# Optimization experiments

Measured on AMD Instinct MI355X. Metric: run time of the kernel, lower is better.

Reference implementation:

```python
import jax, jax.numpy as jnp
import numpy as np

DIM_V = 1024
H = 16
D = DIM_V // H
EPS = 1e-5


def _ln(x, g, b):
    m = jnp.mean(x, axis=-1, keepdims=True)
    v = jnp.var(x, axis=-1, keepdims=True)
    return (x - m) * jax.lax.rsqrt(v + EPS) * g + b


def setup_inputs() -> dict:
    key = jax.random.key(0)
    ks = jax.random.split(key, 8)
    B, Nq, Nk = 4, 1024, 1024
    s = 1.0 / np.sqrt(DIM_V)
    return {
        "Q": jax.random.normal(ks[0], (B, Nq, DIM_V), jnp.float32),
        "K": jax.random.normal(ks[1], (B, Nk, DIM_V), jnp.float32),
        "structure_bias": jax.random.normal(ks[2], (H, B, Nq, Nk), jnp.float32) * 0.1,
        "Wq": jax.random.normal(ks[3], (DIM_V, DIM_V), jnp.float32) * s,
        "bq": jnp.zeros((DIM_V,), jnp.float32),
        "Wk": jax.random.normal(ks[4], (DIM_V, DIM_V), jnp.float32) * s,
        "bk": jnp.zeros((DIM_V,), jnp.float32),
        "Wv": jax.random.normal(ks[5], (DIM_V, DIM_V), jnp.float32) * s,
        "bv": jnp.zeros((DIM_V,), jnp.float32),
        "Wo": jax.random.normal(ks[6], (DIM_V, DIM_V), jnp.float32) * s,
        "bo": jnp.zeros((DIM_V,), jnp.float32),
        "gamma0": jnp.ones((DIM_V,), jnp.float32),
        "beta0": jnp.zeros((DIM_V,), jnp.float32),
        "gamma1": jnp.ones((DIM_V,), jnp.float32),
        "beta1": jnp.zeros((DIM_V,), jnp.float32),
    }


def reference(Q, K, structure_bias, Wq, bq, Wk, bk, Wv, bv, Wo, bo,
              gamma0, beta0, gamma1, beta1):
    B, Nq, _ = Q.shape
    Nk = K.shape[1]
    q = Q @ Wq.T + bq                      # [B,Nq,dV]
    k = K @ Wk.T + bk                      # [B,Nk,dV]
    v = K @ Wv.T + bv                      # [B,Nk,dV]
    # torch cat(split(d_head,2),0) => head-major leading axis; use [H,B,N,D]
    qh = q.reshape(B, Nq, H, D).transpose(2, 0, 1, 3)
    kh = k.reshape(B, Nk, H, D).transpose(2, 0, 1, 3)
    vh = v.reshape(B, Nk, H, D).transpose(2, 0, 1, 3)
    # NOTE: scale by sqrt(dim_V), not sqrt(d_head) — faithful to source
    A = jnp.einsum('hbqd,hbkd->hbqk', qh, kh) / jnp.sqrt(jnp.float32(DIM_V))
    A = jax.nn.softmax(A + structure_bias, axis=-1)
    oh = qh + jnp.einsum('hbqk,hbkd->hbqd', A, vh)   # residual on Q_
    O = oh.transpose(1, 2, 0, 3).reshape(B, Nq, DIM_V)
    O = _ln(O, gamma0, beta0)
    O = O + jax.nn.relu(O @ Wo.T + bo)     # dropout is identity in eval
    O = _ln(O, gamma1, beta1)
    return O
```

## Files before the change

kernel.cpp:

```cpp
#include <hip/hip_runtime.h>

using s8v = __attribute__((ext_vector_type(8))) short;
using s4v = __attribute__((ext_vector_type(4))) short;
using f4v = __attribute__((ext_vector_type(4))) float;
using bf8v = __attribute__((ext_vector_type(8))) __bf16;

__device__ __forceinline__ short f2b(float f) {
  __bf16 h = (__bf16)f;
  return __builtin_bit_cast(short, h);
}

__device__ __forceinline__ f4v mfma16(s8v a, s8v b, f4v c) {
  return __builtin_amdgcn_mfma_f32_16x16x32_bf16(
      __builtin_bit_cast(bf8v, a), __builtin_bit_cast(bf8v, b), c, 0, 0, 0);
}

__device__ __forceinline__ void glds16(const void* src, void* dst) {
  __builtin_amdgcn_global_load_lds(
      (const __attribute__((address_space(1))) void*)src,
      (__attribute__((address_space(3))) void*)dst, 16, 0, 0);
}

__global__ __launch_bounds__(256) void cast_kernel(
    const float* __restrict__ Q, const float* __restrict__ K,
    const float* __restrict__ Wq, const float* __restrict__ Wk,
    const float* __restrict__ Wv, const float* __restrict__ Wo,
    short* __restrict__ Qb, short* __restrict__ Kb,
    short* __restrict__ Wqb, short* __restrict__ Wkb,
    short* __restrict__ Wvb, short* __restrict__ Wob) {
  int bi = blockIdx.x;
  const float* src; short* dst; int off;
  if (bi < 2048)      { src = Q;  dst = Qb;  off = bi; }
  else if (bi < 4096) { src = K;  dst = Kb;  off = bi - 2048; }
  else if (bi < 4608) { src = Wq; dst = Wqb; off = bi - 4096; }
  else if (bi < 5120) { src = Wk; dst = Wkb; off = bi - 4608; }
  else if (bi < 5632) { src = Wv; dst = Wvb; off = bi - 5120; }
  else                { src = Wo; dst = Wob; off = bi - 5632; }
  size_t base = (size_t)off * 2048 + threadIdx.x * 8;
  f4v a = *(const f4v*)(src + base);
  f4v b = *(const f4v*)(src + base + 4);
  s8v o8;
#pragma unroll
  for (int j = 0; j < 4; ++j) { o8[j] = f2b(a[j]); o8[4 + j] = f2b(b[j]); }
  *(s8v*)(dst + base) = o8;
}

__device__ __forceinline__ void gemm_core(const short* __restrict__ A,
                                          const short* __restrict__ W,
                                          f4v acc[4][4], short* As, short* Ws,
                                          int tm, int tn, int tid) {
  const int lane = tid & 63, wid = tid >> 6;
  const int c = lane & 15, g = lane >> 4;
  const int wr = wid >> 1, wc = wid & 1;
  for (int kb = 0; kb < 16; ++kb) {
    __syncthreads();
#pragma unroll
    for (int p = 0; p < 4; ++p) {
      int row = p * 32 + wid * 8 + (lane >> 3);
      int chunk = (lane & 7) ^ (row & 7);
      glds16(A + (size_t)(tm + row) * 1024 + kb * 64 + chunk * 8,
             As + p * 2048 + wid * 512);
      glds16(W + (size_t)(tn + row) * 1024 + kb * 64 + chunk * 8,
             Ws + p * 2048 + wid * 512);
    }
    asm volatile("s_waitcnt vmcnt(0)" ::: "memory");
    __syncthreads();
#pragma unroll
    for (int ks = 0; ks < 2; ++ks) {
      s8v af[4], wf[4];
#pragma unroll
      for (int i = 0; i < 4; ++i) {
        int ra = wr * 64 + i * 16 + c;
        af[i] = *(const s8v*)(As + ra * 64 + ((((ks << 2) + g) ^ (ra & 7)) << 3));
        int rb = wc * 64 + i * 16 + c;
        wf[i] = *(const s8v*)(Ws + rb * 64 + ((((ks << 2) + g) ^ (rb & 7)) << 3));
      }
#pragma unroll
      for (int i = 0; i < 4; ++i)
#pragma unroll
        for (int j = 0; j < 4; ++j)
          acc[i][j] = mfma16(af[i], wf[j], acc[i][j]);
    }
  }
}

__global__ __launch_bounds__(256, 2) void gemm_proj(
    const short* __restrict__ Qb, const short* __restrict__ Kb,
    const short* __restrict__ Wqb, const short* __restrict__ Wkb,
    const short* __restrict__ Wvb, const float* __restrict__ bq,
    const float* __restrict__ bk, const float* __restrict__ bv,
    float* __restrict__ qws, short* __restrict__ khs, short* __restrict__ vts) {
  __shared__ short As[8192], Ws[8192];
  const int tid = threadIdx.x, lane = tid & 63, wid = tid >> 6;
  const int c = lane & 15, g = lane >> 4;
  const int wr = wid >> 1, wc = wid & 1;
  const int tm = blockIdx.y * 128, tn = blockIdx.x * 128;
  const int z = blockIdx.z;
  const short* A = (z == 0) ? Qb : Kb;
  const short* W = (z == 0) ? Wqb : ((z == 1) ? Wkb : Wvb);
  const float* bias = (z == 0) ? bq : ((z == 1) ? bk : bv);
  f4v acc[4][4] = {};
  gemm_core(A, W, acc, As, Ws, tm, tn, tid);
#pragma unroll
  for (int j = 0; j < 4; ++j) {
    const int o = tn + wc * 64 + j * 16 + c;
    const float bj = bias[o];
    const int h = o >> 6, d = o & 63;
#pragma unroll
    for (int i = 0; i < 4; ++i) {
      const int m0 = tm + wr * 64 + i * 16 + g * 4;
      if (z == 0) {
#pragma unroll
        for (int r = 0; r < 4; ++r)
          qws[(size_t)(m0 + r) * 1024 + o] = acc[i][j][r] + bj;
      } else if (z == 1) {
        const int bidx = m0 >> 10;
#pragma unroll
        for (int r = 0; r < 4; ++r) {
          int n = (m0 + r) & 1023;
          khs[((size_t)(h * 4 + bidx) * 1024 + n) * 64 + d] =
              f2b(acc[i][j][r] + bj);
        }
      } else {
        const int bidx = m0 >> 10, n0 = m0 & 1023;
        s4v pk;
#pragma unroll
        for (int r = 0; r < 4; ++r) pk[r] = f2b(acc[i][j][r] + bj);
        *(s4v*)(vts + ((size_t)(h * 4 + bidx) * 64 + d) * 1024 + n0) = pk;
      }
    }
  }
}

__global__ __launch_bounds__(256, 2) void gemm_out(
    const short* __restrict__ t0b, const short* __restrict__ Wob,
    const float* __restrict__ bo, const float* __restrict__ res,
    float* __restrict__ O2) {
  __shared__ short As[8192], Ws[8192];
  const int tid = threadIdx.x, lane = tid & 63, wid = tid >> 6;
  const int c = lane & 15, g = lane >> 4;
  const int wr = wid >> 1, wc = wid & 1;
  const int tm = blockIdx.y * 128, tn = blockIdx.x * 128;
  f4v acc[4][4] = {};
  gemm_core(t0b, Wob, acc, As, Ws, tm, tn, tid);
#pragma unroll
  for (int j = 0; j < 4; ++j) {
    const int o = tn + wc * 64 + j * 16 + c;
    const float bj = bo[o];
#pragma unroll
    for (int i = 0; i < 4; ++i) {
      const int m0 = tm + wr * 64 + i * 16 + g * 4;
#pragma unroll
      for (int r = 0; r < 4; ++r) {
        size_t idx = (size_t)(m0 + r) * 1024 + o;
        float y = acc[i][j][r] + bj;
        y = fmaxf(y, 0.f);
        O2[idx] = res[idx] + y;
      }
    }
  }
}

__global__ __launch_bounds__(256, 2) void attn_kernel(
    const short* __restrict__ khs, const short* __restrict__ vts,
    const float* __restrict__ qf, const float* __restrict__ sb,
    float* __restrict__ o_attn) {
  const int tid = threadIdx.x, wid = tid >> 6, lane = tid & 63;
  const int c = lane & 15, g = lane >> 4;
  const int hb = blockIdx.y, h = hb >> 2, b = hb & 3;
  const int qw = blockIdx.x * 128 + wid * 32;

  __shared__ short Ks[64 * 64];
  __shared__ short Vs[64 * 64];
  __shared__ short Ps[4 * 32 * 72];

  const short* kb_base = khs + (size_t)hb * 65536;
  const short* vb_base = vts + (size_t)hb * 65536;
  const float* sb_base = sb + (size_t)hb * 1048576;

  s8v qb[2][2];
#pragma unroll
  for (int nf = 0; nf < 2; ++nf)
#pragma unroll
    for (int ks = 0; ks < 2; ++ks) {
      const float* qp = qf + ((size_t)(b * 1024 + qw + nf * 16 + c)) * 1024 +
                        h * 64 + ks * 32 + g * 8;
      f4v lo = *(const f4v*)qp;
      f4v hi = *(const f4v*)(qp + 4);
      s8v t;
#pragma unroll
      for (int j = 0; j < 4; ++j) { t[j] = f2b(lo[j]); t[4 + j] = f2b(hi[j]); }
      qb[nf][ks] = t;
    }

  float m_run[2] = {-3.0e38f, -3.0e38f};
  float l_run[2] = {0.f, 0.f};
  f4v oacc[2][4] = {};

  for (int kb = 0; kb < 16; ++kb) {
    __syncthreads();
#pragma unroll
    for (int p = 0; p < 2; ++p) {
      int row = p * 32 + wid * 8 + (lane >> 3);
      int chunk = (lane & 7) ^ (row & 7);
      glds16(kb_base + (size_t)(kb * 64 + row) * 64 + chunk * 8,
             Ks + p * 2048 + wid * 512);
      glds16(vb_base + (size_t)row * 1024 + kb * 64 + chunk * 8,
             Vs + p * 2048 + wid * 512);
    }
    asm volatile("s_waitcnt vmcnt(0)" ::: "memory");
    __syncthreads();

    f4v accs[4][2] = {};
#pragma unroll
    for (int ks = 0; ks < 2; ++ks) {
      s8v kf[4];
#pragma unroll
      for (int mf = 0; mf < 4; ++mf) {
        int row = mf * 16 + c;
        kf[mf] = *(const s8v*)(Ks + row * 64 +
                               ((((ks << 2) + g) ^ (row & 7)) << 3));
      }
#pragma unroll
      for (int mf = 0; mf < 4; ++mf)
#pragma unroll
        for (int nf = 0; nf < 2; ++nf)
          accs[mf][nf] = mfma16(kf[mf], qb[nf][ks], accs[mf][nf]);
    }

    float alpha_s[2];
#pragma unroll
    for (int nf = 0; nf < 2; ++nf) {
      const int q = qw + nf * 16 + c;
      const float* bp0 = sb_base + (size_t)q * 1024 + kb * 64 + g * 4;
      float tmax = -3.0e38f;
#pragma unroll
      for (int mf = 0; mf < 4; ++mf) {
        f4v bb = *(const f4v*)(bp0 + mf * 16);
        f4v x = accs[mf][nf] * 0.03125f + bb;
        accs[mf][nf] = x;
        tmax = fmaxf(tmax, fmaxf(fmaxf(x[0], x[1]), fmaxf(x[2], x[3])));
      }
      tmax = fmaxf(tmax, __shfl_xor(tmax, 16));
      tmax = fmaxf(tmax, __shfl_xor(tmax, 32));
      const float mn = fmaxf(m_run[nf], tmax);
      const float al = __expf(m_run[nf] - mn);
      float ssum = 0.f;
#pragma unroll
      for (int mf = 0; mf < 4; ++mf) {
        f4v x = accs[mf][nf];
        float p0 = __expf(x[0] - mn), p1 = __expf(x[1] - mn);
        float p2 = __expf(x[2] - mn), p3 = __expf(x[3] - mn);
        ssum += (p0 + p1) + (p2 + p3);
        s4v pk;
        pk[0] = f2b(p0); pk[1] = f2b(p1); pk[2] = f2b(p2); pk[3] = f2b(p3);
        *(s4v*)(Ps + (size_t)wid * 2304 + (size_t)(nf * 16 + c) * 72 +
                mf * 16 + g * 4) = pk;
      }
      ssum += __shfl_xor(ssum, 16);
      ssum += __shfl_xor(ssum, 32);
      l_run[nf] = l_run[nf] * al + ssum;
      m_run[nf] = mn;
      alpha_s[nf] = al;
    }

#pragma unroll
    for (int mfq = 0; mfq < 2; ++mfq) {
      float a0 = __shfl(alpha_s[mfq], g * 4 + 0);
      float a1 = __shfl(alpha_s[mfq], g * 4 + 1);
      float a2 = __shfl(alpha_s[mfq], g * 4 + 2);
      float a3 = __shfl(alpha_s[mfq], g * 4 + 3);
#pragma unroll
      for (int nd = 0; nd < 4; ++nd) {
        oacc[mfq][nd][0] *= a0; oacc[mfq][nd][1] *= a1;
        oacc[mfq][nd][2] *= a2; oacc[mfq][nd][3] *= a3;
      }
    }

#pragma unroll
    for (int ks2 = 0; ks2 < 2; ++ks2) {
      s8v pf[2], vf[4];
#pragma unroll
      for (int mfq = 0; mfq < 2; ++mfq)
        pf[mfq] = *(const s8v*)(Ps + (size_t)wid * 2304 +
                                (size_t)(mfq * 16 + c) * 72 + ks2 * 32 + g * 8);
#pragma unroll
      for (int nd = 0; nd < 4; ++nd) {
        int d = nd * 16 + c;
        vf[nd] = *(const s8v*)(Vs + d * 64 +
                               ((((ks2 << 2) + g) ^ (d & 7)) << 3));
      }
#pragma unroll
      for (int mfq = 0; mfq < 2; ++mfq)
#pragma unroll
        for (int nd = 0; nd < 4; ++nd)
          oacc[mfq][nd] = mfma16(pf[mfq], vf[nd], oacc[mfq][nd]);
    }
  }

#pragma unroll
  for (int mfq = 0; mfq < 2; ++mfq) {
    float i0 = 1.f / __shfl(l_run[mfq], g * 4 + 0);
    float i1 = 1.f / __shfl(l_run[mfq], g * 4 + 1);
    float i2 = 1.f / __shfl(l_run[mfq], g * 4 + 2);
    float i3 = 1.f / __shfl(l_run[mfq], g * 4 + 3);
#pragma unroll
    for (int nd = 0; nd < 4; ++nd) {
      int d = nd * 16 + c;
      size_t base = ((size_t)(b * 1024 + qw + mfq * 16 + g * 4)) * 1024 +
                    h * 64 + d;
      o_attn[base]        = qf[base]        + oacc[mfq][nd][0] * i0;
      o_attn[base + 1024] = qf[base + 1024] + oacc[mfq][nd][1] * i1;
      o_attn[base + 2048] = qf[base + 2048] + oacc[mfq][nd][2] * i2;
      o_attn[base + 3072] = qf[base + 3072] + oacc[mfq][nd][3] * i3;
    }
  }
}

template <bool WB>
__global__ __launch_bounds__(256) void ln_k(const float* __restrict__ in,
                                            float* __restrict__ out,
                                            short* __restrict__ outb,
                                            const float* __restrict__ gamma,
                                            const float* __restrict__ beta) {
  const int row = blockIdx.x, tid = threadIdx.x;
  const size_t base = (size_t)row * 1024 + tid * 4;
  f4v x = *(const f4v*)(in + base);
  float s = (x[0] + x[1]) + (x[2] + x[3]);
  float ss = (x[0] * x[0] + x[1] * x[1]) + (x[2] * x[2] + x[3] * x[3]);
#pragma unroll
  for (int m = 1; m < 64; m <<= 1) {
    s += __shfl_xor(s, m);
    ss += __shfl_xor(ss, m);
  }
  __shared__ float red[8];
  const int wid = tid >> 6, lane = tid & 63;
  if (lane == 0) { red[wid] = s; red[4 + wid] = ss; }
  __syncthreads();
  s = (red[0] + red[1]) + (red[2] + red[3]);
  ss = (red[4] + red[5]) + (red[6] + red[7]);
  const float mean = s * (1.f / 1024.f);
  const float var = ss * (1.f / 1024.f) - mean * mean;
  const float rs = rsqrtf(var + 1e-5f);
  const f4v gg = *(const f4v*)(gamma + tid * 4);
  const f4v bb = *(const f4v*)(beta + tid * 4);
  f4v y;
#pragma unroll
  for (int jj = 0; jj < 4; ++jj) y[jj] = (x[jj] - mean) * rs * gg[jj] + bb[jj];
  *(f4v*)(out + base) = y;
  if (WB) {
    s4v pk;
#pragma unroll
    for (int jj = 0; jj < 4; ++jj) pk[jj] = f2b(y[jj]);
    *(s4v*)(outb + base) = pk;
  }
}

extern "C" void kernel_launch(void* const* d_in, const int* in_sizes, int n_in,
                              void* d_out, int out_size, void* d_ws,
                              size_t ws_size, hipStream_t stream) {
  const float* Q  = (const float*)d_in[0];
  const float* K  = (const float*)d_in[1];
  const float* sb = (const float*)d_in[2];
  const float* Wq = (const float*)d_in[3];
  const float* bq = (const float*)d_in[4];
  const float* Wk = (const float*)d_in[5];
  const float* bk = (const float*)d_in[6];
  const float* Wv = (const float*)d_in[7];
  const float* bv = (const float*)d_in[8];
  const float* Wo = (const float*)d_in[9];
  const float* bo = (const float*)d_in[10];
  const float* g0 = (const float*)d_in[11];
  const float* b0 = (const float*)d_in[12];
  const float* g1 = (const float*)d_in[13];
  const float* b1 = (const float*)d_in[14];
  float* out = (float*)d_out;

  char* ws = (char*)d_ws;
  size_t off = 0;
  auto alloc = [&](size_t bytes) -> void* {
    void* p = ws + off;
    off += (bytes + 255) & ~(size_t)255;
    return p;
  };
  float* qws  = (float*)alloc((size_t)16 << 20);
  short* khs  = (short*)alloc((size_t)8 << 20);
  short* vts  = (short*)alloc((size_t)8 << 20);
  short* Qb   = (short*)alloc((size_t)8 << 20);
  short* Kb   = (short*)alloc((size_t)8 << 20);
  short* Wqb  = (short*)alloc((size_t)2 << 20);
  short* Wkb  = (short*)alloc((size_t)2 << 20);
  short* Wvb  = (short*)alloc((size_t)2 << 20);
  short* Wob  = (short*)alloc((size_t)2 << 20);
  float* oat  = (float*)alloc((size_t)16 << 20);
  short* t0b  = (short*)alloc((size_t)8 << 20);
  float* O2   = qws;

  cast_kernel<<<6144, 256, 0, stream>>>(Q, K, Wq, Wk, Wv, Wo, Qb, Kb, Wqb, Wkb,
                                        Wvb, Wob);
  gemm_proj<<<dim3(8, 32, 3), 256, 0, stream>>>(Qb, Kb, Wqb, Wkb, Wvb, bq, bk,
                                                bv, qws, khs, vts);
  attn_kernel<<<dim3(8, 64), 256, 0, stream>>>(khs, vts, qws, sb, oat);
  ln_k<true><<<4096, 256, 0, stream>>>(oat, oat, t0b, g0, b0);
  gemm_out<<<dim3(8, 32), 256, 0, stream>>>(t0b, Wob, bo, oat, O2);
  ln_k<false><<<4096, 256, 0, stream>>>(O2, out, nullptr, g1, b1);
}
```

Measured before the change: 543.8 us.

## Double-buffer LDS tiles in GEMMs and attention, prefetch bias, remap blocks across XCDs

GEMM and attention kernels now double-buffer their LDS tiles, issuing the next tile's global-to-LDS loads before computing on the current tile. The attention kernel also prefetches the next structure-bias block into registers. Block indices are remapped so neighbouring tiles land on the same XCD for better L2 reuse. This targets exposed global memory latency, at the cost of more LDS and registers per block, which may lower occupancy.

Result: faster. 529.5 us (-2.6%).

```diff
diff --git a/kernel.cpp b/kernel.cpp
--- a/kernel.cpp
+++ b/kernel.cpp
@@ -45,43 +45,65 @@
   *(s8v*)(dst + base) = o8;
 }
 
-__device__ __forceinline__ void gemm_core(const short* __restrict__ A,
-                                          const short* __restrict__ W,
-                                          f4v acc[4][4], short* As, short* Ws,
-                                          int tm, int tn, int tid) {
+__device__ __forceinline__ void stage_tile(const short* __restrict__ A,
+                                           const short* __restrict__ W,
+                                           short* As, short* Ws, int tm, int tn,
+                                           int kb, int tid) {
+  const int lane = tid & 63, wid = tid >> 6;
+#pragma unroll
+  for (int p = 0; p < 4; ++p) {
+    int row = p * 32 + wid * 8 + (lane >> 3);
+    int chunk = (lane & 7) ^ (row & 7);
+    glds16(A + (size_t)(tm + row) * 1024 + kb * 64 + chunk * 8,
+           As + p * 2048 + wid * 512);
+    glds16(W + (size_t)(tn + row) * 1024 + kb * 64 + chunk * 8,
+           Ws + p * 2048 + wid * 512);
+  }
+}
+
+__device__ __forceinline__ void gemm_core_db(const short* __restrict__ A,
+                                             const short* __restrict__ W,
+                                             f4v acc[4][4], short* As, short* Ws,
+                                             int tm, int tn, int tid) {
   const int lane = tid & 63, wid = tid >> 6;
   const int c = lane & 15, g = lane >> 4;
   const int wr = wid >> 1, wc = wid & 1;
+  stage_tile(A, W, As, Ws, tm, tn, 0, tid);
+  asm volatile("s_waitcnt vmcnt(0)" ::: "memory");
+  __syncthreads();
   for (int kb = 0; kb < 16; ++kb) {
-    __syncthreads();
-#pragma unroll
-    for (int p = 0; p < 4; ++p) {
-      int row = p * 32 + wid * 8 + (lane >> 3);
-      int chunk = (lane & 7) ^ (row & 7);
-      glds16(A + (size_t)(tm + row) * 1024 + kb * 64 + chunk * 8,
-             As + p * 2048 + wid * 512);
-      glds16(W + (size_t)(tn + row) * 1024 + kb * 64 + chunk * 8,
-             Ws + p * 2048 + wid * 512);
+    const int cur = kb & 1;
+    short* Asc = As + cur * 8192;
+    short* Wsc = Ws + cur * 8192;
+    if (kb < 15)
+      stage_tile(A, W, As + (cur ^ 1) * 8192, Ws + (cur ^ 1) * 8192, tm, tn,
+                 kb + 1, tid);
+#pragma unroll
+    for (int ks = 0; ks < 2; ++ks) {
+      s8v af[4], wf[4];
+#pragma unroll
+      for (int i = 0; i < 4; ++i) {
+        int ra = wr * 64 + i * 16 + c;
+        af[i] = *(const s8v*)(Asc + ra * 64 + ((((ks << 2) + g) ^ (ra & 7)) << 3));
+        int rb = wc * 64 + i * 16 + c;
+        wf[i] = *(const s8v*)(Wsc + rb * 64 + ((((ks << 2) + g) ^ (rb & 7)) << 3));
+      }
+#pragma unroll
+      for (int i = 0; i < 4; ++i)
+#pragma unroll
+        for (int j = 0; j < 4; ++j)
+          acc[i][j] = mfma16(af[i], wf[j], acc[i][j]);
     }
     asm volatile("s_waitcnt vmcnt(0)" ::: "memory");
     __syncthreads();
-#pragma unroll
-    for (int ks = 0; ks < 2; ++ks) {
-      s8v af[4], wf[4];
-#pragma unroll
-      for (int i = 0; i < 4; ++i) {
-        int ra = wr * 64 + i * 16 + c;
-        af[i] = *(const s8v*)(As + ra * 64 + ((((ks << 2) + g) ^ (ra & 7)) << 3));
-        int rb = wc * 64 + i * 16 + c;
-        wf[i] = *(const s8v*)(Ws + rb * 64 + ((((ks << 2) + g) ^ (rb & 7)) << 3));
-      }
-#pragma unroll
-      for (int i = 0; i < 4; ++i)
-#pragma unroll
-        for (int j = 0; j < 4; ++j)
-          acc[i][j] = mfma16(af[i], wf[j], acc[i][j]);
-    }
-  }
+  }
+}
+
+__device__ __forceinline__ void xcd_remap_gemm(int* tm, int* tn) {
+  int d = blockIdx.y * 8 + blockIdx.x;
+  int o = (d & 7) * 32 + (d >> 3);
+  *tm = (o >> 3) * 128;
+  *tn = (o & 7) * 128;
 }
 
 __global__ __launch_bounds__(256, 2) void gemm_proj(
@@ -90,17 +112,18 @@
     const short* __restrict__ Wvb, const float* __restrict__ bq,
     const float* __restrict__ bk, const float* __restrict__ bv,
     float* __restrict__ qws, short* __restrict__ khs, short* __restrict__ vts) {
-  __shared__ short As[8192], Ws[8192];
+  __shared__ short As[16384], Ws[16384];
   const int tid = threadIdx.x, lane = tid & 63, wid = tid >> 6;
   const int c = lane & 15, g = lane >> 4;
   const int wr = wid >> 1, wc = wid & 1;
-  const int tm = blockIdx.y * 128, tn = blockIdx.x * 128;
+  int tm, tn;
+  xcd_remap_gemm(&tm, &tn);
   const int z = blockIdx.z;
   const short* A = (z == 0) ? Qb : Kb;
   const short* W = (z == 0) ? Wqb : ((z == 1) ? Wkb : Wvb);
   const float* bias = (z == 0) ? bq : ((z == 1) ? bk : bv);
   f4v acc[4][4] = {};
-  gemm_core(A, W, acc, As, Ws, tm, tn, tid);
+  gemm_core_db(A, W, acc, As, Ws, tm, tn, tid);
 #pragma unroll
   for (int j = 0; j < 4; ++j) {
     const int o = tn + wc * 64 + j * 16 + c;
@@ -136,13 +159,14 @@
     const short* __restrict__ t0b, const short* __restrict__ Wob,
     const float* __restrict__ bo, const float* __restrict__ res,
     float* __restrict__ O2) {
-  __shared__ short As[8192], Ws[8192];
+  __shared__ short As[16384], Ws[16384];
   const int tid = threadIdx.x, lane = tid & 63, wid = tid >> 6;
   const int c = lane & 15, g = lane >> 4;
   const int wr = wid >> 1, wc = wid & 1;
-  const int tm = blockIdx.y * 128, tn = blockIdx.x * 128;
+  int tm, tn;
+  xcd_remap_gemm(&tm, &tn);
   f4v acc[4][4] = {};
-  gemm_core(t0b, Wob, acc, As, Ws, tm, tn, tid);
+  gemm_core_db(t0b, Wob, acc, As, Ws, tm, tn, tid);
 #pragma unroll
   for (int j = 0; j < 4; ++j) {
     const int o = tn + wc * 64 + j * 16 + c;
@@ -167,11 +191,13 @@
     float* __restrict__ o_attn) {
   const int tid = threadIdx.x, wid = tid >> 6, lane = tid & 63;
   const int c = lane & 15, g = lane >> 4;
-  const int hb = blockIdx.y, h = hb >> 2, b = hb & 3;
-  const int qw = blockIdx.x * 128 + wid * 32;
-
-  __shared__ short Ks[64 * 64];
-  __shared__ short Vs[64 * 64];
+  const int dlin = blockIdx.y * 8 + blockIdx.x;
+  const int o = (dlin & 7) * 64 + (dlin >> 3);
+  const int hb = o >> 3, h = hb >> 2, b = hb & 3;
+  const int qw = (o & 7) * 128 + wid * 32;
+
+  __shared__ short Ks[2 * 4096];
+  __shared__ short Vs[2 * 4096];
   __shared__ short Ps[4 * 32 * 72];
 
   const short* kb_base = khs + (size_t)hb * 65536;
@@ -193,23 +219,49 @@
       qb[nf][ks] = t;
     }
 
-  float m_run[2] = {-3.0e38f, -3.0e38f};
-  float l_run[2] = {0.f, 0.f};
-  f4v oacc[2][4] = {};
-
-  for (int kb = 0; kb < 16; ++kb) {
-    __syncthreads();
+  auto stage_kv = [&](int buf, int kb) {
 #pragma unroll
     for (int p = 0; p < 2; ++p) {
       int row = p * 32 + wid * 8 + (lane >> 3);
       int chunk = (lane & 7) ^ (row & 7);
       glds16(kb_base + (size_t)(kb * 64 + row) * 64 + chunk * 8,
-             Ks + p * 2048 + wid * 512);
+             Ks + buf * 4096 + p * 2048 + wid * 512);
       glds16(vb_base + (size_t)row * 1024 + kb * 64 + chunk * 8,
-             Vs + p * 2048 + wid * 512);
-    }
-    asm volatile("s_waitcnt vmcnt(0)" ::: "memory");
-    __syncthreads();
+             Vs + buf * 4096 + p * 2048 + wid * 512);
+    }
+  };
+
+  float m_run[2] = {-3.0e38f, -3.0e38f};
+  float l_run[2] = {0.f, 0.f};
+  f4v oacc[2][4] = {};
+
+  stage_kv(0, 0);
+  f4v bc[2][4];
+#pragma unroll
+  for (int nf = 0; nf < 2; ++nf) {
+    const float* bp0 =
+        sb_base + (size_t)(qw + nf * 16 + c) * 1024 + g * 4;
+#pragma unroll
+    for (int mf = 0; mf < 4; ++mf) bc[nf][mf] = *(const f4v*)(bp0 + mf * 16);
+  }
+  asm volatile("s_waitcnt vmcnt(0)" ::: "memory");
+  __syncthreads();
+
+  for (int kb = 0; kb < 16; ++kb) {
+    const int cur = kb & 1;
+    const short* Ksc = Ks + cur * 4096;
+    const short* Vsc = Vs + cur * 4096;
+    if (kb < 15) stage_kv(cur ^ 1, kb + 1);
+    f4v bn[2][4];
+    if (kb < 15) {
+#pragma unroll
+      for (int nf = 0; nf < 2; ++nf) {
+        const float* bp0 = sb_base + (size_t)(qw + nf * 16 + c) * 1024 +
+                           (kb + 1) * 64 + g * 4;
+#pragma unroll
+        for (int mf = 0; mf < 4; ++mf) bn[nf][mf] = *(const f4v*)(bp0 + mf * 16);
+      }
+    }
 
     f4v accs[4][2] = {};
 #pragma unroll
@@ -218,7 +270,7 @@
 #pragma unroll
       for (int mf = 0; mf < 4; ++mf) {
         int row = mf * 16 + c;
-        kf[mf] = *(const s8v*)(Ks + row * 64 +
+        kf[mf] = *(const s8v*)(Ksc + row * 64 +
                                ((((ks << 2) + g) ^ (row & 7)) << 3));
       }
 #pragma unroll
@@ -231,13 +283,10 @@
     float alpha_s[2];
 #pragma unroll
     for (int nf = 0; nf < 2; ++nf) {
-      const int q = qw + nf * 16 + c;
-      const float* bp0 = sb_base + (size_t)q * 1024 + kb * 64 + g * 4;
       float tmax = -3.0e38f;
 #pragma unroll
       for (int mf = 0; mf < 4; ++mf) {
-        f4v bb = *(const f4v*)(bp0 + mf * 16);
-        f4v x = accs[mf][nf] * 0.03125f + bb;
+        f4v x = accs[mf][nf] * 0.03125f + bc[nf][mf];
         accs[mf][nf] = x;
         tmax = fmaxf(tmax, fmaxf(fmaxf(x[0], x[1]), fmaxf(x[2], x[3])));
       }
@@ -287,7 +336,7 @@
 #pragma unroll
       for (int nd = 0; nd < 4; ++nd) {
         int d = nd * 16 + c;
-        vf[nd] = *(const s8v*)(Vs + d * 64 +
+        vf[nd] = *(const s8v*)(Vsc + d * 64 +
                                ((((ks2 << 2) + g) ^ (d & 7)) << 3));
       }
 #pragma unroll
@@ -295,6 +344,15 @@
 #pragma unroll
         for (int nd = 0; nd < 4; ++nd)
           oacc[mfq][nd] = mfma16(pf[mfq], vf[nd], oacc[mfq][nd]);
+    }
+
+    asm volatile("s_waitcnt vmcnt(0)" ::: "memory");
+    __syncthreads();
+    if (kb < 15) {
+#pragma unroll
+      for (int nf = 0; nf < 2; ++nf)
+#pragma unroll
+        for (int mf = 0; mf < 4; ++mf) bc[nf][mf] = bn[nf][mf];
     }
   }
 
```
